# Kernel tuning notes

Hardware: AMD Instinct MI355X
Metric: run time of the kernel (lower is better)

The kernel has to match this reference:

```python
import jax, jax.numpy as jnp
import numpy as np

B, N = 256, 2000          # clouds, points per cloud
M1, M2 = 100, 5           # fps sample counts (ratio 0.05 twice)
K1, K2 = 20, 20           # neighbors per cluster (= 1/ratio)
R1, R2, R3 = 0.3, 1.0, 2.0
F1, F2, F3 = 5, 25, 45


def _fps(pts, m):
    # iterative farthest point sampling, deterministic start at index 0
    n = pts.shape[0]
    def step(carry, _):
        mind, last = carry
        d = jnp.sum((pts - pts[last]) ** 2, axis=-1)
        mind = jnp.minimum(mind, d)
        return (mind, jnp.argmax(mind).astype(jnp.int32)), last
    _, idx = jax.lax.scan(step, (jnp.full((n,), 1e10, pts.dtype), jnp.int32(0)), None, length=m)
    return idx


def _radius_knn(q, pts, k, r):
    # k nearest neighbors of each query, masked to the radius ball (static-shape gnn.radius)
    d = jnp.sum((q[:, None, :] - pts[None, :, :]) ** 2, axis=-1)  # (M, n)
    negd, idx = jax.lax.top_k(-d, k)
    return idx, (-negd) <= r * r


def _masked_max(h, mask):
    return jnp.max(jnp.where(mask[..., None], h, -1e10), axis=1)


def _forward(points, W1, b1, W2, b2, W3, b3, D1, bD1, D2, bD2, D3, bD3):
    def per_cloud(pts):
        # ---- encode level 1 ----
        samples = pts[_fps(pts, M1)]                              # (M1,3)
        idx1, m1 = _radius_knn(samples, pts, K1, R1)
        rel = (pts[idx1] - samples[:, None, :]) / R1 * m1[..., None]   # (M1,K1,3)
        f1 = _masked_max(jax.nn.relu(rel @ W1 + b1), m1)          # (M1,F1)
        # ---- encode level 2 ----
        samples2 = samples[_fps(samples, M2)]                     # (M2,3)
        idx2, m2 = _radius_knn(samples2, samples, K2, R2)
        rel2 = (samples[idx2] - samples2[:, None, :]) / R2 * m2[..., None]
        h2 = jax.nn.relu(jnp.concatenate([rel2, f1[idx2]], axis=-1) @ W2 + b2)
        f2 = _masked_max(h2, m2)                                  # (M2,F2)
        # ---- encode level 3 (global) ----
        rel3 = samples2 / R3
        h3 = jax.nn.relu(jnp.concatenate([rel3, f2], axis=-1) @ W3 + b3)
        latent = jnp.max(h3, axis=0)                              # (F3,)
        # ---- hierarchical decode ----
        o1 = (latent @ D1 + bD1).reshape(M2, 3 + F2)
        dec, cf = o1[:, :3], jax.nn.relu(o1[:, 3:])               # (M2,3),(M2,F2)
        o2 = (cf @ D2 + bD2).reshape(M2 * K2, 3 + F1)
        dec2, cf2 = o2[:, :3], jax.nn.relu(o2[:, 3:])             # (M2*K2,3/F1)
        dec3 = (cf2 @ D3 + bD3).reshape(M2 * K2 * K1, 3)
        # ---- reconstruction: repeat_interleave + add + scale ----
        s2_out = dec * R3
        s_out = (jnp.repeat(s2_out, K2, axis=0) + dec2) * R2
        return (jnp.repeat(s_out, K1, axis=0) + dec3) * R1        # (N,3)
    return jax.vmap(per_cloud)(points).reshape(B * N, 3)


def setup_inputs():
    key = jax.random.key(0)
    ks = jax.random.split(key, 8)
    p = lambda k, s: jax.random.normal(k, s, jnp.float32) * 0.1
    z = lambda s: jnp.zeros((s,), jnp.float32)
    return {
        "points": jax.random.normal(ks[0], (B, N, 3), jnp.float32),
        "W1": p(ks[1], (3, F1)), "b1": z(F1),
        "W2": p(ks[2], (3 + F1, F2)), "b2": z(F2),
        "W3": p(ks[3], (3 + F2, F3)), "b3": z(F3),
        "D1": p(ks[4], (F3, M2 * (3 + F2))), "bD1": z(M2 * (3 + F2)),
        "D2": p(ks[5], (F2, K2 * (3 + F1))), "bD2": z(K2 * (3 + F1)),
        "D3": p(ks[6], (F1, K1 * 3)), "bD3": z(K1 * 3),
    }


def reference(points, W1, b1, W2, b2, W3, b3, D1, bD1, D2, bD2, D3, bD3):
    return _forward(points, W1, b1, W2, b2, W3, b3, D1, bD1, D2, bD2, D3, bD3)
```

## Files before the change

kernel.cpp:

```cpp
#include <hip/hip_runtime.h>

#define TPB 256
#define NW 4
#define NPTS 2000
#define M1C 100
#define M2C 5
#define KNN 20
#define CANDCAP 128
#define PCH 32

typedef float v2f __attribute__((ext_vector_type(2)));

__device__ __forceinline__ float dist3(float px, float py, float pz,
                                       float qx, float qy, float qz) {
#pragma clang fp contract(off)
    float dx = px - qx, dy = py - qy, dz = pz - qz;
    return dx * dx + dy * dy + dz * dz;
}

__device__ __forceinline__ v2f dist3p(v2f px, v2f py, v2f pz, v2f q0, v2f q1, v2f q2) {
#pragma clang fp contract(off)
    v2f dx = px - q0, dy = py - q1, dz = pz - q2;
    v2f ax = dx * dx;
    v2f ay = dy * dy;
    v2f az = dz * dz;
    return (ax + ay) + az;
}

#define ARGMAX_STEP(ctrl, rm)                                                        \
    do {                                                                             \
        float ov = __int_as_float(__builtin_amdgcn_update_dpp(                       \
            (int)0xff800000, __float_as_int(v), ctrl, rm, 0xf, false));              \
        int oi = __builtin_amdgcn_update_dpp(0x7fffffff, i, ctrl, rm, 0xf, false);   \
        bool take = (ov > v) || (ov == v && oi < i);                                 \
        v = take ? ov : v;                                                           \
        i = take ? oi : i;                                                           \
    } while (0)

__device__ __forceinline__ void wave_argmax(float& v, int& i) {
    ARGMAX_STEP(0x111, 0xf);
    ARGMAX_STEP(0x112, 0xf);
    ARGMAX_STEP(0x114, 0xf);
    ARGMAX_STEP(0x118, 0xf);
    ARGMAX_STEP(0x142, 0xa);
    ARGMAX_STEP(0x143, 0xc);
    v = __int_as_float(__builtin_amdgcn_readlane(__float_as_int(v), 63));
    i = __builtin_amdgcn_readlane(i, 63);
}

#define FMAX_STEP(ctrl, rm)                                                          \
    do {                                                                             \
        float _t = __int_as_float(__builtin_amdgcn_update_dpp(                       \
            (int)0xff800000, __float_as_int(x), ctrl, rm, 0xf, false));              \
        x = fmaxf(x, _t);                                                            \
    } while (0)

__device__ __forceinline__ float wave_fmax(float x) {
    FMAX_STEP(0x111, 0xf);
    FMAX_STEP(0x112, 0xf);
    FMAX_STEP(0x114, 0xf);
    FMAX_STEP(0x118, 0xf);
    FMAX_STEP(0x142, 0xa);
    FMAX_STEP(0x143, 0xc);
    return __int_as_float(__builtin_amdgcn_readlane(__float_as_int(x), 63));
}

#define PTS16(X) X(0) X(1) X(2) X(3) X(4) X(5) X(6) X(7) \
                 X(8) X(9) X(10) X(11) X(12) X(13) X(14) X(15)

__global__ __launch_bounds__(TPB, 1) void fused_kernel(
    const float* __restrict__ P,
    const float* __restrict__ W1, const float* __restrict__ b1,
    const float* __restrict__ W2, const float* __restrict__ b2,
    const float* __restrict__ W3, const float* __restrict__ b3,
    const float* __restrict__ D1, const float* __restrict__ bD1,
    const float* __restrict__ D2, const float* __restrict__ bD2,
    const float* __restrict__ D3, const float* __restrict__ bD3,
    float* __restrict__ out)
{
    __shared__ float sx[NPTS], sy[NPTS], sz[NPTS];
    __shared__ float smpx[M1C], smpy[M1C], smpz[M1C];
    __shared__ float s2x[M2C], s2y[M2C], s2z[M2C];
    __shared__ float f1s[M1C][5];
    __shared__ float knd[NW][CANDCAP];
    __shared__ int   kni[NW][CANDCAP];
    __shared__ float vin[M2C][KNN][8];
    __shared__ int prog;
    __shared__ float f2s[M2C][25];
    __shared__ float latent[45];
    __shared__ float decv[M2C][3];
    __shared__ float cfs[M2C][25];
    __shared__ float dec2s[M1C][3];
    __shared__ float cf2s[M1C][5];
    __shared__ float w2s[200], b2s[25], w3s[1260], b3s[45];

    const int b = blockIdx.x;
    const int tid = threadIdx.x;
    const int lane = tid & 63;
    const int wid = tid >> 6;

    const float R1SQ = (float)(0.3 * 0.3);
    const float R2SQ = 1.0f;
    const float INVR1 = 1.0f / 0.3f;

    const float* Pb = P + (size_t)b * (NPTS * 3);
    for (int j = tid; j < NPTS; j += TPB) {
        sx[j] = Pb[3 * j + 0];
        sy[j] = Pb[3 * j + 1];
        sz[j] = Pb[3 * j + 2];
    }
    for (int t = tid; t < 200; t += TPB) w2s[t] = W2[t];
    for (int t = tid; t < 25; t += TPB) b2s[t] = b2[t];
    for (int t = tid; t < 1260; t += TPB) w3s[t] = W3[t];
    for (int t = tid; t < 45; t += TPB) b3s[t] = b3[t];
    if (tid == 0) prog = -1;
    __syncthreads();

    if (wid == 0) {
#define DECLP(p) v2f px##p, py##p, pz##p, mind##p;
        PTS16(DECLP)
#undef DECLP

#define INITP(p) {                                                        \
        const int j0 = (2*(p)) * 64 + lane;                               \
        const int j1 = (2*(p)+1) * 64 + lane;                             \
        const bool v0 = j0 < NPTS, v1 = j1 < NPTS;                        \
        const int a0 = v0 ? j0 : 0, a1 = v1 ? j1 : 0;                     \
        px##p[0] = v0 ? sx[a0] : 1e18f;  px##p[1] = v1 ? sx[a1] : 1e18f;  \
        py##p[0] = v0 ? sy[a0] : 1e18f;  py##p[1] = v1 ? sy[a1] : 1e18f;  \
        pz##p[0] = v0 ? sz[a0] : 1e18f;  pz##p[1] = v1 ? sz[a1] : 1e18f;  \
        mind##p[0] = v0 ? 1e10f : -1.0f; mind##p[1] = v1 ? 1e10f : -1.0f; \
    }
        PTS16(INITP)
#undef INITP

        float qx = sx[0], qy = sy[0], qz = sz[0];
        for (int it = 0; it < M1C; ++it) {
            if (lane == 0) {
                smpx[it] = qx; smpy[it] = qy; smpz[it] = qz;
                __hip_atomic_store(&prog, it, __ATOMIC_RELEASE,
                                   __HIP_MEMORY_SCOPE_WORKGROUP);
            }
            if (it == M1C - 1) break;

            v2f q0 = {qx, qx}, q1 = {qy, qy}, q2 = {qz, qz};
            float bv[4] = {-1e30f, -1e30f, -1e30f, -1e30f};
            int   bk[4] = {0, 0, 0, 0};
#define STEPP(p) {                                                        \
        v2f d = dist3p(px##p, py##p, pz##p, q0, q1, q2);                  \
        v2f mm;                                                           \
        mm[0] = fminf(mind##p[0], d[0]);                                  \
        mm[1] = fminf(mind##p[1], d[1]);                                  \
        mind##p = mm;                                                     \
        { const int c0 = 2*(p), s0 = c0 & 3;                              \
          bool t0 = mm[0] > bv[s0];                                       \
          bv[s0] = t0 ? mm[0] : bv[s0];                                   \
          bk[s0] = t0 ? c0 : bk[s0]; }                                    \
        { const int c1 = 2*(p)+1, s1 = c1 & 3;                            \
          bool t1 = mm[1] > bv[s1];                                       \
          bv[s1] = t1 ? mm[1] : bv[s1];                                   \
          bk[s1] = t1 ? c1 : bk[s1]; }                                    \
    }
            PTS16(STEPP)
#undef STEPP
            float V = bv[0]; int K = bk[0];
            {
                bool t = (bv[1] > V) || (bv[1] == V && bk[1] < K);
                V = t ? bv[1] : V; K = t ? bk[1] : K;
            }
            {
                bool t = (bv[2] > V) || (bv[2] == V && bk[2] < K);
                V = t ? bv[2] : V; K = t ? bk[2] : K;
            }
            {
                bool t = (bv[3] > V) || (bv[3] == V && bk[3] < K);
                V = t ? bv[3] : V; K = t ? bk[3] : K;
            }
            float bvv = V;
            int bi = (K << 6) | lane;
            wave_argmax(bvv, bi);
            qx = sx[bi]; qy = sy[bi]; qz = sz[bi];
        }

        {
            float ax = smpx[lane], ay = smpy[lane], az = smpz[lane];
            bool vb2 = lane < (M1C - 64);
            float bx2 = vb2 ? smpx[lane + 64] : 1e18f;
            float by2 = vb2 ? smpy[lane + 64] : 1e18f;
            float bz2 = vb2 ? smpz[lane + 64] : 1e18f;
            float m2a = 1e10f;
            float m2b = vb2 ? 1e10f : -1.0f;
            int last2 = 0;
            for (int it = 0; it < M2C; ++it) {
                float fx = smpx[last2], fy = smpy[last2], fz = smpz[last2];
                if (lane == 0) { s2x[it] = fx; s2y[it] = fy; s2z[it] = fz; }
                m2a = fminf(m2a, dist3(ax, ay, az, fx, fy, fz));
                m2b = fminf(m2b, dist3(bx2, by2, bz2, fx, fy, fz));
                float v = m2a; int i = lane;
                if (m2b > v) { v = m2b; i = lane + 64; }
                wave_argmax(v, i);
                last2 = i;
            }
        }
    } else {
        float rw1[15], rb1[5];
#pragma unroll
        for (int i = 0; i < 15; ++i) rw1[i] = W1[i];
#pragma unroll
        for (int i = 0; i < 5; ++i) rb1[i] = b1[i];

        for (int s = wid - 1; s < M1C; s += (NW - 1)) {
            while (__hip_atomic_load(&prog, __ATOMIC_ACQUIRE,
                                     __HIP_MEMORY_SCOPE_WORKGROUP) < s)
                __builtin_amdgcn_s_sleep(1);
            float qx = smpx[s], qy = smpy[s], qz = smpz[s];
            int cn = 0;
#pragma unroll 4
            for (int c = 0; c < 32; ++c) {
                int j = c * 64 + lane;
                float d = 0.0f; bool pred = false;
                if (j < NPTS) {
                    d = dist3(sx[j], sy[j], sz[j], qx, qy, qz);
                    pred = (d <= R1SQ);
                }
                unsigned long long mb = __ballot(pred);
                if (pred) {
                    int pos = cn + (int)__popcll(mb & ((1ull << lane) - 1ull));
                    if (pos < CANDCAP) { knd[wid][pos] = d; kni[wid][pos] = j; }
                }
                cn += (int)__popcll(mb);
            }
            if (cn > CANDCAP) cn = CANDCAP;
            float fmx[5];
#pragma unroll
            for (int f = 0; f < 5; ++f) fmx[f] = -1e30f;
            for (int t = lane; t < cn; t += 64) {
                float d = knd[wid][t]; int j = kni[wid][t];
                bool valid = true;
                if (cn > KNN) {
                    int rank = 0;
                    for (int u = 0; u < cn; ++u) {
                        float du = knd[wid][u]; int iu = kni[wid][u];
                        rank += (du < d || (du == d && iu < j)) ? 1 : 0;
                    }
                    valid = rank < KNN;
                }
                if (valid) {
                    float rx = (sx[j] - qx) * INVR1;
                    float ry = (sy[j] - qy) * INVR1;
                    float rz = (sz[j] - qz) * INVR1;
#pragma unroll
                    for (int f = 0; f < 5; ++f) {
                        float h = fmaf(rx, rw1[f], fmaf(ry, rw1[5 + f], fmaf(rz, rw1[10 + f], rb1[f])));
                        fmx[f] = fmaxf(fmx[f], fmaxf(h, 0.0f));
                    }
                }
            }
#pragma unroll
            for (int f = 0; f < 5; ++f) fmx[f] = wave_fmax(fmx[f]);
            if (lane == 0) {
#pragma unroll
                for (int f = 0; f < 5; ++f) f1s[s][f] = fmx[f];
            }
        }
    }
    __syncthreads();

    for (int s = wid; s < M2C; s += NW) {
        float qx2 = s2x[s], qy2 = s2y[s], qz2 = s2z[s];
        int cn = 0;
#pragma unroll
        for (int c = 0; c < 2; ++c) {
            int j = c * 64 + lane;
            float d = 0.0f; bool pred = false;
            if (j < M1C) {
                d = dist3(smpx[j], smpy[j], smpz[j], qx2, qy2, qz2);
                pred = (d <= R2SQ);
            }
            unsigned long long mb = __ballot(pred);
            if (pred) {
                int pos = cn + (int)__popcll(mb & ((1ull << lane) - 1ull));
                knd[wid][pos] = d; kni[wid][pos] = j;
            }
            cn += (int)__popcll(mb);
        }
        int nv = 0;
#pragma unroll
        for (int c = 0; c < 2; ++c) {
            int t = c * 64 + lane;
            bool valid = false;
            float in8[8];
            if (t < cn) {
                float d = knd[wid][t]; int j = kni[wid][t];
                valid = true;
                if (cn > KNN) {
                    int rank = 0;
                    for (int u = 0; u < cn; ++u) {
                        float du = knd[wid][u]; int iu = kni[wid][u];
                        rank += (du < d || (du == d && iu < j)) ? 1 : 0;
                    }
                    valid = rank < KNN;
                }
                if (valid) {
                    in8[0] = smpx[j] - qx2; in8[1] = smpy[j] - qy2; in8[2] = smpz[j] - qz2;
#pragma unroll
                    for (int f = 0; f < 5; ++f) in8[3 + f] = f1s[j][f];
                }
            }
            unsigned long long mb = __ballot(valid);
            if (valid) {
                int pos = nv + (int)__popcll(mb & ((1ull << lane) - 1ull));
#pragma unroll
                for (int i = 0; i < 8; ++i) vin[s][pos][i] = in8[i];
            }
            nv += (int)__popcll(mb);
        }
        if (lane < 25) {
            float hmx = -1e30f;
            for (int c = 0; c < nv; ++c) {
                float h = b2s[lane];
#pragma unroll
                for (int i = 0; i < 8; ++i) h = fmaf(vin[s][c][i], w2s[i * 25 + lane], h);
                hmx = fmaxf(hmx, fmaxf(h, 0.0f));
            }
            f2s[s][lane] = hmx;
        }
    }
    __syncthreads();

    if (wid == 0 && lane < 45) {
        float lm = -1e30f;
        for (int r = 0; r < M2C; ++r) {
            float h = b3s[lane];
            h = fmaf(s2x[r] * 0.5f, w3s[0 * 45 + lane], h);
            h = fmaf(s2y[r] * 0.5f, w3s[1 * 45 + lane], h);
            h = fmaf(s2z[r] * 0.5f, w3s[2 * 45 + lane], h);
#pragma unroll
            for (int i = 0; i < 25; ++i) h = fmaf(f2s[r][i], w3s[(3 + i) * 45 + lane], h);
            lm = fmaxf(lm, fmaxf(h, 0.0f));
        }
        latent[lane] = lm;
    }
    __syncthreads();

    for (int t = tid; t < 140; t += TPB) {
        float acc = bD1[t];
        for (int i = 0; i < 45; i++) acc = fmaf(latent[i], D1[i * 140 + t], acc);
        int r = t / 28, c = t % 28;
        if (c < 3) decv[r][c] = acc;
        else cfs[r][c - 3] = fmaxf(acc, 0.0f);
    }
    __syncthreads();

    for (int t = tid; t < 800; t += TPB) {
        int r = t / 160, c = t % 160;
        float acc = bD2[c];
        for (int i = 0; i < 25; i++) acc = fmaf(cfs[r][i], D2[i * 160 + c], acc);
        int g = r * 20 + c / 8, c8 = c % 8;
        if (c8 < 3) dec2s[g][c8] = acc;
        else cf2s[g][c8 - 3] = fmaxf(acc, 0.0f);
    }
    __syncthreads();

    float* outb = out + (size_t)b * (NPTS * 3);
    for (int t = tid; t < NPTS * 3; t += TPB) {
        int n = t / 3, c = t % 3;
        int g = n / 20;
        int m = n / 400;
        int r60 = (n % 20) * 3 + c;
        float acc = bD3[r60];
        for (int i = 0; i < 5; i++) acc = fmaf(cf2s[g][i], D3[i * 60 + r60], acc);
        float val = ((decv[m][c] * 2.0f + dec2s[g][c]) + acc) * 0.3f;
        outb[t] = val;
    }
}

extern "C" void kernel_launch(void* const* d_in, const int* in_sizes, int n_in,
                              void* d_out, int out_size, void* d_ws, size_t ws_size,
                              hipStream_t stream) {
    const float* P   = (const float*)d_in[0];
    const float* W1  = (const float*)d_in[1];
    const float* b1  = (const float*)d_in[2];
    const float* W2  = (const float*)d_in[3];
    const float* b2  = (const float*)d_in[4];
    const float* W3  = (const float*)d_in[5];
    const float* b3  = (const float*)d_in[6];
    const float* D1  = (const float*)d_in[7];
    const float* bD1 = (const float*)d_in[8];
    const float* D2  = (const float*)d_in[9];
    const float* bD2 = (const float*)d_in[10];
    const float* D3  = (const float*)d_in[11];
    const float* bD3 = (const float*)d_in[12];
    float* out = (float*)d_out;

    int B = in_sizes[0] / (NPTS * 3);
    hipLaunchKernelGGL(fused_kernel, dim3(B), dim3(TPB), 0, stream,
                       P, W1, b1, W2, b2, W3, b3, D1, bD1, D2, bD2, D3, bD3, out);
}
```

Baseline: 205.7 us.

## Pack points as float4 in LDS and let FPS wave handle tail kNN queries

Point coordinates move from three separate LDS arrays into one float4 array, so each point is fetched with a single vector LDS load. The level-1 radius/kNN work is split: worker waves take queries below KSPLIT, and the FPS wave handles the last few queries itself once sampling finishes. The goal is to shorten the tail where the final queries could only start after the last FPS sample was published. An empty asm barrier also pins the per-point FPS registers. LDS footprint for the points grows by a third, and the split point is a hand-tuned constant.

```diff
diff --git a/kernel.cpp b/kernel.cpp
--- a/kernel.cpp
+++ b/kernel.cpp
@@ -7,7 +7,7 @@
 #define M2C 5
 #define KNN 20
 #define CANDCAP 128
-#define PCH 32
+#define KSPLIT 95
 
 typedef float v2f __attribute__((ext_vector_type(2)));
 
@@ -78,7 +78,7 @@
     const float* __restrict__ D3, const float* __restrict__ bD3,
     float* __restrict__ out)
 {
-    __shared__ float sx[NPTS], sy[NPTS], sz[NPTS];
+    __shared__ __align__(16) float4 sp[NPTS];
     __shared__ float smpx[M1C], smpy[M1C], smpz[M1C];
     __shared__ float s2x[M2C], s2y[M2C], s2z[M2C];
     __shared__ float f1s[M1C][5];
@@ -105,9 +105,7 @@
 
     const float* Pb = P + (size_t)b * (NPTS * 3);
     for (int j = tid; j < NPTS; j += TPB) {
-        sx[j] = Pb[3 * j + 0];
-        sy[j] = Pb[3 * j + 1];
-        sz[j] = Pb[3 * j + 2];
+        sp[j] = make_float4(Pb[3 * j + 0], Pb[3 * j + 1], Pb[3 * j + 2], 0.0f);
     }
     for (int t = tid; t < 200; t += TPB) w2s[t] = W2[t];
     for (int t = tid; t < 25; t += TPB) b2s[t] = b2[t];
@@ -116,25 +114,83 @@
     if (tid == 0) prog = -1;
     __syncthreads();
 
+#define KNN1_BODY(S, ROW) {                                                       \
+        float qx = smpx[S], qy = smpy[S], qz = smpz[S];                           \
+        int cn = 0;                                                               \
+        _Pragma("unroll 4")                                                       \
+        for (int c = 0; c < 32; ++c) {                                            \
+            int j = c * 64 + lane;                                                \
+            float d = 0.0f; bool pred = false;                                    \
+            if (j < NPTS) {                                                       \
+                float4 pj = sp[j];                                                \
+                d = dist3(pj.x, pj.y, pj.z, qx, qy, qz);                          \
+                pred = (d <= R1SQ);                                               \
+            }                                                                     \
+            unsigned long long mb = __ballot(pred);                               \
+            if (pred) {                                                           \
+                int pos = cn + (int)__popcll(mb & ((1ull << lane) - 1ull));       \
+                if (pos < CANDCAP) { knd[ROW][pos] = d; kni[ROW][pos] = j; }      \
+            }                                                                     \
+            cn += (int)__popcll(mb);                                              \
+        }                                                                         \
+        if (cn > CANDCAP) cn = CANDCAP;                                           \
+        float fmx[5];                                                             \
+        _Pragma("unroll")                                                         \
+        for (int f = 0; f < 5; ++f) fmx[f] = -1e30f;                              \
+        for (int t = lane; t < cn; t += 64) {                                     \
+            float d = knd[ROW][t]; int j = kni[ROW][t];                           \
+            bool valid = true;                                                    \
+            if (cn > KNN) {                                                       \
+                int rank = 0;                                                     \
+                for (int u = 0; u < cn; ++u) {                                    \
+                    float du = knd[ROW][u]; int iu = kni[ROW][u];                 \
+                    rank += (du < d || (du == d && iu < j)) ? 1 : 0;              \
+                }                                                                 \
+                valid = rank < KNN;                                               \
+            }                                                                     \
+            if (valid) {                                                          \
+                float4 pj = sp[j];                                                \
+                float rx = (pj.x - qx) * INVR1;                                   \
+                float ry = (pj.y - qy) * INVR1;                                   \
+                float rz = (pj.z - qz) * INVR1;                                   \
+                _Pragma("unroll")                                                 \
+                for (int f = 0; f < 5; ++f) {                                     \
+                    float h = fmaf(rx, rw1[f],                                    \
+                              fmaf(ry, rw1[5 + f],                               \
+                              fmaf(rz, rw1[10 + f], rb1[f])));                    \
+                    fmx[f] = fmaxf(fmx[f], fmaxf(h, 0.0f));                       \
+                }                                                                 \
+            }                                                                     \
+        }                                                                         \
+        _Pragma("unroll")                                                         \
+        for (int f = 0; f < 5; ++f) fmx[f] = wave_fmax(fmx[f]);                   \
+        if (lane == 0) {                                                          \
+            _Pragma("unroll")                                                     \
+            for (int f = 0; f < 5; ++f) f1s[S][f] = fmx[f];                       \
+        }                                                                         \
+    }
+
     if (wid == 0) {
 #define DECLP(p) v2f px##p, py##p, pz##p, mind##p;
         PTS16(DECLP)
 #undef DECLP
 
-#define INITP(p) {                                                        \
-        const int j0 = (2*(p)) * 64 + lane;                               \
-        const int j1 = (2*(p)+1) * 64 + lane;                             \
-        const bool v0 = j0 < NPTS, v1 = j1 < NPTS;                        \
-        const int a0 = v0 ? j0 : 0, a1 = v1 ? j1 : 0;                     \
-        px##p[0] = v0 ? sx[a0] : 1e18f;  px##p[1] = v1 ? sx[a1] : 1e18f;  \
-        py##p[0] = v0 ? sy[a0] : 1e18f;  py##p[1] = v1 ? sy[a1] : 1e18f;  \
-        pz##p[0] = v0 ? sz[a0] : 1e18f;  pz##p[1] = v1 ? sz[a1] : 1e18f;  \
-        mind##p[0] = v0 ? 1e10f : -1.0f; mind##p[1] = v1 ? 1e10f : -1.0f; \
+#define INITP(p) {                                                          \
+        const int j0_ = (2*(p)) * 64 + lane;                                \
+        const int j1_ = (2*(p)+1) * 64 + lane;                              \
+        const bool v0_ = j0_ < NPTS, v1_ = j1_ < NPTS;                      \
+        const float4 A_ = sp[v0_ ? j0_ : 0];                                \
+        const float4 B_ = sp[v1_ ? j1_ : 0];                                \
+        px##p[0] = v0_ ? A_.x : 1e18f;  px##p[1] = v1_ ? B_.x : 1e18f;      \
+        py##p[0] = v0_ ? A_.y : 1e18f;  py##p[1] = v1_ ? B_.y : 1e18f;      \
+        pz##p[0] = v0_ ? A_.z : 1e18f;  pz##p[1] = v1_ ? B_.z : 1e18f;      \
+        mind##p[0] = v0_ ? 1e10f : -1.0f; mind##p[1] = v1_ ? 1e10f : -1.0f; \
     }
         PTS16(INITP)
 #undef INITP
 
-        float qx = sx[0], qy = sy[0], qz = sz[0];
+        float4 qq0 = sp[0];
+        float qx = qq0.x, qy = qq0.y, qz = qq0.z;
         for (int it = 0; it < M1C; ++it) {
             if (lane == 0) {
                 smpx[it] = qx; smpy[it] = qy; smpz[it] = qz;
@@ -146,20 +202,22 @@
             v2f q0 = {qx, qx}, q1 = {qy, qy}, q2 = {qz, qz};
             float bv[4] = {-1e30f, -1e30f, -1e30f, -1e30f};
             int   bk[4] = {0, 0, 0, 0};
-#define STEPP(p) {                                                        \
-        v2f d = dist3p(px##p, py##p, pz##p, q0, q1, q2);                  \
-        v2f mm;                                                           \
-        mm[0] = fminf(mind##p[0], d[0]);                                  \
-        mm[1] = fminf(mind##p[1], d[1]);                                  \
-        mind##p = mm;                                                     \
-        { const int c0 = 2*(p), s0 = c0 & 3;                              \
-          bool t0 = mm[0] > bv[s0];                                       \
-          bv[s0] = t0 ? mm[0] : bv[s0];                                   \
-          bk[s0] = t0 ? c0 : bk[s0]; }                                    \
-        { const int c1 = 2*(p)+1, s1 = c1 & 3;                            \
-          bool t1 = mm[1] > bv[s1];                                       \
-          bv[s1] = t1 ? mm[1] : bv[s1];                                   \
-          bk[s1] = t1 ? c1 : bk[s1]; }                                    \
+#define STEPP(p) {                                                          \
+        v2f d = dist3p(px##p, py##p, pz##p, q0, q1, q2);                    \
+                      \
+        asm volatile("" : "+v"(px##p), "+v"(py##p), "+v"(pz##p));           \
+        v2f mm;                                                             \
+        mm[0] = fminf(mind##p[0], d[0]);                                    \
+        mm[1] = fminf(mind##p[1], d[1]);                                    \
+        mind##p = mm;                                                       \
+        { const int c0 = 2*(p), s0 = c0 & 3;                                \
+          bool t0 = mm[0] > bv[s0];                                         \
+          bv[s0] = t0 ? mm[0] : bv[s0];                                     \
+          bk[s0] = t0 ? c0 : bk[s0]; }                                      \
+        { const int c1 = 2*(p)+1, s1 = c1 & 3;                              \
+          bool t1 = mm[1] > bv[s1];                                         \
+          bv[s1] = t1 ? mm[1] : bv[s1];                                     \
+          bk[s1] = t1 ? c1 : bk[s1]; }                                      \
     }
             PTS16(STEPP)
 #undef STEPP
@@ -179,7 +237,8 @@
             float bvv = V;
             int bi = (K << 6) | lane;
             wave_argmax(bvv, bi);
-            qx = sx[bi]; qy = sy[bi]; qz = sz[bi];
+            float4 qq = sp[bi];
+            qx = qq.x; qy = qq.y; qz = qq.z;
         }
 
         {
@@ -202,6 +261,15 @@
                 last2 = i;
             }
         }
+
+        {
+            float rw1[15], rb1[5];
+#pragma unroll
+            for (int i = 0; i < 15; ++i) rw1[i] = W1[i];
+#pragma unroll
+            for (int i = 0; i < 5; ++i) rb1[i] = b1[i];
+            for (int s = KSPLIT; s < M1C; ++s) KNN1_BODY(s, 0);
+        }
     } else {
         float rw1[15], rb1[5];
 #pragma unroll
@@ -209,59 +277,11 @@
 #pragma unroll
         for (int i = 0; i < 5; ++i) rb1[i] = b1[i];
 
-        for (int s = wid - 1; s < M1C; s += (NW - 1)) {
+        for (int s = wid - 1; s < KSPLIT; s += (NW - 1)) {
             while (__hip_atomic_load(&prog, __ATOMIC_ACQUIRE,
                                      __HIP_MEMORY_SCOPE_WORKGROUP) < s)
                 __builtin_amdgcn_s_sleep(1);
-            float qx = smpx[s], qy = smpy[s], qz = smpz[s];
-            int cn = 0;
-#pragma unroll 4
-            for (int c = 0; c < 32; ++c) {
-                int j = c * 64 + lane;
-                float d = 0.0f; bool pred = false;
-                if (j < NPTS) {
-                    d = dist3(sx[j], sy[j], sz[j], qx, qy, qz);
-                    pred = (d <= R1SQ);
-                }
-                unsigned long long mb = __ballot(pred);
-                if (pred) {
-                    int pos = cn + (int)__popcll(mb & ((1ull << lane) - 1ull));
-                    if (pos < CANDCAP) { knd[wid][pos] = d; kni[wid][pos] = j; }
-                }
-                cn += (int)__popcll(mb);
-            }
-            if (cn > CANDCAP) cn = CANDCAP;
-            float fmx[5];
-#pragma unroll
-            for (int f = 0; f < 5; ++f) fmx[f] = -1e30f;
-            for (int t = lane; t < cn; t += 64) {
-                float d = knd[wid][t]; int j = kni[wid][t];
-                bool valid = true;
-                if (cn > KNN) {
-                    int rank = 0;
-                    for (int u = 0; u < cn; ++u) {
-                        float du = knd[wid][u]; int iu = kni[wid][u];
-                        rank += (du < d || (du == d && iu < j)) ? 1 : 0;
-                    }
-                    valid = rank < KNN;
-                }
-                if (valid) {
-                    float rx = (sx[j] - qx) * INVR1;
-                    float ry = (sy[j] - qy) * INVR1;
-                    float rz = (sz[j] - qz) * INVR1;
-#pragma unroll
-                    for (int f = 0; f < 5; ++f) {
-                        float h = fmaf(rx, rw1[f], fmaf(ry, rw1[5 + f], fmaf(rz, rw1[10 + f], rb1[f])));
-                        fmx[f] = fmaxf(fmx[f], fmaxf(h, 0.0f));
-                    }
-                }
-            }
-#pragma unroll
-            for (int f = 0; f < 5; ++f) fmx[f] = wave_fmax(fmx[f]);
-            if (lane == 0) {
-#pragma unroll
-                for (int f = 0; f < 5; ++f) f1s[s][f] = fmx[f];
-            }
+            KNN1_BODY(s, wid);
         }
     }
     __syncthreads();
```

Result: slower. 239.6 us (+16.5%).
